# Kernel tuning notes

Measured on AMD Instinct MI355X. Metric: run time of the kernel, lower is better.

The kernel has to match this reference:

```python
import jax, jax.numpy as jnp
import numpy as np

B = 2; CIN = 64; COUT = 64; H = 192; W = 192
KH = 3; KW = 3; K = KH * KW; NC = 20
STRIDE = 1; PAD = 1; DIL = 1


def setup_inputs() -> dict:
    key = jax.random.key(0)
    ks = jax.random.split(key, 7)
    x = jax.random.normal(ks[0], (B, CIN, H, W), jnp.float32)
    input_LO = jax.random.uniform(ks[1], (B, NC, H, W), jnp.float32)
    output_LO = jax.random.uniform(ks[2], (B, NC, H, W), jnp.float32)  # HO=H, WO=W for k3 s1 p1
    weight = jax.random.normal(ks[3], (COUT, CIN, KH, KW), jnp.float32) * 0.05
    bias = jax.random.normal(ks[4], (COUT,), jnp.float32) * 0.05
    # conv_offset is zero-init in source; use small random weights so offsets are exercised
    off_w = jax.random.normal(ks[5], (2 * K, CIN, KH, KW), jnp.float32) * 0.01
    off_b = jnp.zeros((2 * K,), jnp.float32)
    return {"x": x, "input_LO": input_LO, "output_LO": output_LO,
            "weight": weight, "bias": bias, "off_w": off_w, "off_b": off_b}


def _gather(img_flat, idx):
    # img_flat: [B, C, H*W], idx: [B, N] -> [B, C, N]
    return jax.vmap(lambda im, ix: im[:, ix])(img_flat, idx)


def _bilinear(img, py, px, zero_pad):
    """Bilinear sample img [B,C,Hi,Wi] at pixel coords py/px [B,K,Ho,Wo].
    zero_pad=True -> zeros outside (deformable conv); False -> border clamp (grid_sample border)."""
    Bb, Cc, Hh, Ww = img.shape
    if not zero_pad:
        px = jnp.clip(px, 0.0, Ww - 1.0)
        py = jnp.clip(py, 0.0, Hh - 1.0)
    x0 = jnp.floor(px)
    y0 = jnp.floor(py)
    img_f = img.reshape(Bb, Cc, Hh * Ww)
    out = jnp.zeros((Bb, Cc) + px.shape[1:], img.dtype)
    for dy in (0.0, 1.0):
        for dx in (0.0, 1.0):
            yc = y0 + dy
            xc = x0 + dx
            w = (1.0 - jnp.abs(py - yc)) * (1.0 - jnp.abs(px - xc))
            if zero_pad:
                valid = (yc >= 0) & (yc <= Hh - 1) & (xc >= 0) & (xc <= Ww - 1)
                w = w * valid.astype(w.dtype)
            yi = jnp.clip(yc, 0, Hh - 1).astype(jnp.int32)
            xi = jnp.clip(xc, 0, Ww - 1).astype(jnp.int32)
            idx = (yi * Ww + xi).reshape(Bb, -1)
            g = _gather(img_f, idx).reshape((Bb, Cc) + px.shape[1:])
            out = out + g * w[:, None]
    return out


def reference(x, input_LO, output_LO, weight, bias, off_w, off_b):
    # 1) offset conv (torch chunk+cat is identity, so offset == conv_offset(x))
    offset = jax.lax.conv_general_dilated(
        x, off_w, (STRIDE, STRIDE), ((PAD, PAD), (PAD, PAD)),
        dimension_numbers=("NCHW", "OIHW", "NCHW")) + off_b[None, :, None, None]
    Bb, _, Ho, Wo = offset.shape
    off = offset.reshape(Bb, K, 2, Ho, Wo)
    off_y = off[:, :, 0]   # channel 2k   -> y offset
    off_x = off[:, :, 1]   # channel 2k+1 -> x offset
    hk = (jnp.arange(K) // KW).astype(x.dtype)[None, :, None, None]
    wk = (jnp.arange(K) % KW).astype(x.dtype)[None, :, None, None]

    # 2) mask: grid_sample label map at deformed locations (align_corners=True, border pad)
    hor = jnp.linspace(-1.0, 1.0, Wo)[None, None, None, :]
    ver = jnp.linspace(-1.0, 1.0, Ho)[None, None, :, None]
    gx = hor * STRIDE - PAD + (wk + off_x) / ((W - 1.0) / 2.0)
    gy = ver * STRIDE - PAD + (hk + off_y) / ((H - 1.0) / 2.0)
    px = (gx + 1.0) * (W - 1.0) / 2.0
    py = (gy + 1.0) * (H - 1.0) / 2.0
    samp_LO = _bilinear(input_LO, py, px, zero_pad=False)        # [B,NC,K,Ho,Wo]
    mask = jnp.einsum("bnkhw,bnhw->bkhw", samp_LO, output_LO)    # [B,K,Ho,Wo]

    # 3) modulated deformable conv (DCNv2 math, zero padding outside)
    base_y = (jnp.arange(Ho) * STRIDE - PAD).astype(x.dtype)[None, None, :, None]
    base_x = (jnp.arange(Wo) * STRIDE - PAD).astype(x.dtype)[None, None, None, :]
    py2 = base_y + hk * DIL + off_y
    px2 = base_x + wk * DIL + off_x
    samp = _bilinear(x, py2, px2, zero_pad=True)                 # [B,C,K,Ho,Wo]
    samp = samp * mask[:, None]
    out = jnp.einsum("bckhw,ock->bohw", samp, weight.reshape(COUT, CIN, K))
    return out + bias[None, :, None, None]
```

## Files before the change

### kernel.cpp

```cpp
#include <hip/hip_runtime.h>
#include <hip/hip_fp16.h>

#define Bn   2
#define CIN  64
#define COUT 64
#define Hd   192
#define Wd   192
#define HWd  (Hd*Wd)
#define Kk   9
#define NCh  20
#define NCP  24
#define NTILE 1152

typedef __attribute__((ext_vector_type(8))) short short8;
typedef __attribute__((ext_vector_type(4))) float f32x4;

static __device__ __forceinline__ ushort f2bf(float f) {
    unsigned u = __float_as_uint(f);
    u += 0x7fffu + ((u >> 16) & 1u);
    return (ushort)(u >> 16);
}
static __device__ __forceinline__ float bf2f(ushort v) {
    return __uint_as_float(((unsigned)v) << 16);
}
static __device__ __forceinline__ ushort f2h(float f) {
    return __half_as_ushort(__float2half_rn(f));
}
static __device__ __forceinline__ float h2f(ushort u) {
    return __half2float(__ushort_as_half(u));
}

__global__ __launch_bounds__(256) void kT(const float* __restrict__ x,
        const float* __restrict__ inLO, const float* __restrict__ outLO,
        const float* __restrict__ w, const float* __restrict__ off_w,
        ushort* __restrict__ xtb, ushort* __restrict__ inLOb,
        ushort* __restrict__ outLOb, ushort* __restrict__ wtb,
        ushort* __restrict__ owtb) {
    __shared__ float lds[20 * 257];
    int bid = blockIdx.x, tid = threadIdx.x;
    if (bid < 1152) {
        int b = bid / 576, p0 = (bid % 576) * 64;
        const float* src = x + b * CIN * HWd + p0;
        #pragma unroll
        for (int r = 0; r < 16; ++r) {
            int e = r * 256 + tid;
            int c = e >> 6, p = e & 63;
            lds[c * 65 + p] = src[c * HWd + p];
        }
        __syncthreads();
        ushort* dst = xtb + ((size_t)(b * HWd + p0)) * 64;
        #pragma unroll
        for (int r = 0; r < 16; ++r) {
            int e = r * 256 + tid;
            int p = e >> 6, c = e & 63;
            dst[e] = f2bf(lds[c * 65 + p]);
        }
    } else if (bid < 1728) {
        int q = bid - 1152;
        int t = q / 288; q %= 288;
        int b = q / 144, p0 = (q % 144) * 256;
        const float* src = (t == 0 ? inLO : outLO) + b * NCh * HWd + p0;
        ushort* dst = (t == 0 ? inLOb : outLOb) + ((size_t)(b * HWd + p0)) * NCP;
        #pragma unroll
        for (int r = 0; r < 20; ++r) {
            int e = r * 256 + tid;
            int n = e >> 8, p = e & 255;
            lds[n * 257 + p] = src[n * HWd + p];
        }
        __syncthreads();
        #pragma unroll
        for (int r = 0; r < 24; ++r) {
            int e = r * 256 + tid;
            int p = e / NCP, n = e - p * NCP;
            dst[e] = (n < NCh) ? f2bf(lds[n * 257 + p]) : (ushort)0;
        }
    } else if (bid < 1872) {
        int f = (bid - 1728) * 256 + tid;
        int e = f & 7, lane = (f >> 3) & 63;
        int kt = (f >> 9) & 1, nt = (f >> 10) & 3, tap = f >> 12;
        int o = nt * 16 + (lane & 15);
        int c = kt * 32 + (lane >> 4) * 8 + e;
        wtb[f] = f2bf(w[(o * CIN + c) * Kk + tap]);
    } else {
        int f = (bid - 1872) * 256 + tid;
        if (f < 18432) {
            int e = f & 7, lane = (f >> 3) & 63;
            int kt = (f >> 9) & 1, nt = (f >> 10) & 1, tap = f >> 11;
            int oc = nt * 16 + (lane & 15);
            int c = kt * 32 + (lane >> 4) * 8 + e;
            owtb[f] = (oc < 18) ? f2bf(off_w[(oc * CIN + c) * Kk + tap]) : (ushort)0;
        }
    }
}

__global__ __launch_bounds__(256) void k1_gemm(const ushort* __restrict__ xtb,
        const ushort* __restrict__ owtb, const float* __restrict__ off_b,
        float* __restrict__ off) {
    int tid = threadIdx.x, bid = blockIdx.x;
    int jt = bid % 3, i = (bid / 3) % Hd, b = bid / (3 * Hd);
    int j0 = jt * 64;
    int lane = tid & 63, wv = tid >> 6;
    int m = lane & 15;
    int ch8 = lane >> 4;
    int j = j0 + wv * 16 + m;
    const ushort* xb = xtb + (size_t)b * HWd * 64;

    float bv0 = off_b[m];
    float bv1 = (m < 2) ? off_b[16 + m] : 0.f;
    f32x4 acc0 = (f32x4){bv0, bv0, bv0, bv0};
    f32x4 acc1 = (f32x4){bv1, bv1, bv1, bv1};
    short8 zero8 = {0, 0, 0, 0, 0, 0, 0, 0};

    #pragma unroll
    for (int t = 0; t < 9; ++t) {
        int yy = i + t / 3 - 1;
        int xx = j + t % 3 - 1;
        bool ok = (yy >= 0) && (yy < Hd) && (xx >= 0) && (xx < Wd);
        int yc = min(max(yy, 0), Hd - 1), xc = min(max(xx, 0), Wd - 1);
        const ushort* rowp = xb + (size_t)(yc * Wd + xc) * 64 + ch8 * 8;
        short8 a0 = *(const short8*)rowp;
        short8 a1 = *(const short8*)(rowp + 32);
        a0 = ok ? a0 : zero8;
        a1 = ok ? a1 : zero8;
        const ushort* wb = owtb + ((size_t)t << 11);
        short8 b00 = *(const short8*)(wb + (lane << 3));
        short8 b01 = *(const short8*)(wb + 512 + (lane << 3));
        short8 b10 = *(const short8*)(wb + 1024 + (lane << 3));
        short8 b11 = *(const short8*)(wb + 1536 + (lane << 3));
        acc0 = __builtin_amdgcn_mfma_f32_16x16x32_bf16(a0, b00, acc0, 0, 0, 0);
        acc0 = __builtin_amdgcn_mfma_f32_16x16x32_bf16(a1, b01, acc0, 0, 0, 0);
        acc1 = __builtin_amdgcn_mfma_f32_16x16x32_bf16(a0, b10, acc1, 0, 0, 0);
        acc1 = __builtin_amdgcn_mfma_f32_16x16x32_bf16(a1, b11, acc1, 0, 0, 0);
    }

    int prow = j0 + wv * 16 + (lane >> 4) * 4;
    int oc = lane & 15;
    float* ob = off + (size_t)b * 18 * HWd + i * Wd;
    #pragma unroll
    for (int r = 0; r < 4; ++r)
        ob[oc * HWd + prow + r] = acc0[r];
    if (oc < 2) {
        #pragma unroll
        for (int r = 0; r < 4; ++r)
            ob[(16 + oc) * HWd + prow + r] = acc1[r];
    }
}

__global__ __launch_bounds__(256) void k2_mask(const ushort* __restrict__ inLOb,
        const ushort* __restrict__ outLOb, const float* __restrict__ off,
        uint4* __restrict__ rec) {
    int t = blockIdx.x * 256 + threadIdx.x;
    int p = t % HWd;
    int k = (t / HWd) % Kk;
    int b = t / (Kk * HWd);
    int j = p % Wd, i = p / Wd;
    float offy = off[(b * 18 + 2 * k) * HWd + p];
    float offx = off[(b * 18 + 2 * k + 1) * HWd + p];

    float py = (float)(i + (k / 3)) + offy - 95.5f;
    float px = (float)(j + (k % 3)) + offx - 95.5f;
    py = fminf(fmaxf(py, 0.f), 191.f);
    px = fminf(fmaxf(px, 0.f), 191.f);
    float y0f = floorf(py), x0f = floorf(px);
    float ly = py - y0f, lx = px - x0f;
    int y0 = (int)y0f, x0 = (int)x0f;
    int y1 = min(y0 + 1, Hd - 1), x1 = min(x0 + 1, Wd - 1);
    float w00 = (1.f - ly) * (1.f - lx);
    float w01 = (1.f - ly) * lx;
    float w10 = ly * (1.f - lx);
    float w11 = ly * lx;
    const short8* L00 = (const short8*)(inLOb + (size_t)(b * HWd + y0 * Wd + x0) * NCP);
    const short8* L01 = (const short8*)(inLOb + (size_t)(b * HWd + y0 * Wd + x1) * NCP);
    const short8* L10 = (const short8*)(inLOb + (size_t)(b * HWd + y1 * Wd + x0) * NCP);
    const short8* L11 = (const short8*)(inLOb + (size_t)(b * HWd + y1 * Wd + x1) * NCP);
    const short8* O  = (const short8*)(outLOb + (size_t)(b * HWd + p) * NCP);
    float acc = 0.f;
    #pragma unroll
    for (int n3 = 0; n3 < 3; ++n3) {
        short8 a = L00[n3], bb = L01[n3], c = L10[n3], d = L11[n3], o = O[n3];
        #pragma unroll
        for (int e = 0; e < 8; ++e) {
            float s = w00 * bf2f((ushort)a[e]) + w01 * bf2f((ushort)bb[e])
                    + w10 * bf2f((ushort)c[e]) + w11 * bf2f((ushort)d[e]);
            acc += s * bf2f((ushort)o[e]);
        }
    }

    float py2 = (float)(i - 1 + (k / 3)) + offy;
    float px2 = (float)(j - 1 + (k % 3)) + offx;
    float y0f2 = floorf(py2), x0f2 = floorf(px2);
    float ly2 = py2 - y0f2, lx2 = px2 - x0f2;
    int yA = (int)y0f2, xA = (int)x0f2;
    int yB = yA + 1, xB = xA + 1;
    bool vy0 = (yA >= 0 && yA < Hd), vy1 = (yB >= 0 && yB < Hd);
    bool vx0 = (xA >= 0 && xA < Wd), vx1 = (xB >= 0 && xB < Wd);
    float W00 = (vy0 && vx0) ? (1.f - ly2) * (1.f - lx2) * acc : 0.f;
    float W01 = (vy0 && vx1) ? (1.f - ly2) * lx2 * acc : 0.f;
    float W10 = (vy1 && vx0) ? ly2 * (1.f - lx2) * acc : 0.f;
    float W11 = (vy1 && vx1) ? ly2 * lx2 * acc : 0.f;
    int y0c = min(max(yA, 0), Hd - 1), y1c = min(max(yB, 0), Hd - 1);
    int x0c = min(max(xA, 0), Wd - 1), x1c = min(max(xB, 0), Wd - 1);
    uint4 r;
    r.x = (unsigned)y0c | ((unsigned)y1c << 16);
    r.y = (unsigned)x0c | ((unsigned)x1c << 16);
    r.z = (unsigned)f2h(W00) | ((unsigned)f2h(W01) << 16);
    r.w = (unsigned)f2h(W10) | ((unsigned)f2h(W11) << 16);
    rec[(size_t)(b * Kk + k) * HWd + p] = r;
}

__global__ __launch_bounds__(256) void k3_part(const ushort* __restrict__ xtb,
        const uint4* __restrict__ rec, const ushort* __restrict__ wtb,
        ushort* __restrict__ part) {
    __shared__ __align__(16) ushort A_lds[4 * 2 * 64 * 8];
    int tid = threadIdx.x;
    int bid = blockIdx.x;
    int h = bid >= NTILE;
    int tb = bid - (h ? NTILE : 0);
    int t0 = h ? 5 : 0, t1 = h ? 9 : 5;
    int jt = tb % 3, i = (tb / 3) % Hd, b = tb / (3 * Hd);
    int j0 = jt * 64;

    int lane = tid & 63;
    int wv_id = tid >> 6;
    int wm = wv_id >> 1;
    int wn = wv_id & 1;

    int pxo = lane & 7;
    int chunk = lane >> 3;
    int kt_s = chunk >> 2;
    int ksub = chunk & 3;
    const ushort* xb = xtb + (size_t)b * HWd * 64;

    f32x4 acc[2][2];
    #pragma unroll
    for (int mi = 0; mi < 2; ++mi)
        #pragma unroll
        for (int ni = 0; ni < 2; ++ni)
            acc[mi][ni] = (f32x4){0.f, 0.f, 0.f, 0.f};

    for (int t = t0; t < t1; ++t) {
        short8 bf[2][2];
        #pragma unroll
        for (int kt = 0; kt < 2; ++kt)
            #pragma unroll
            for (int ni = 0; ni < 2; ++ni) {
                int nt = wn * 2 + ni;
                bf[kt][ni] = *(const short8*)(wtb +
                    ((((t * 4 + nt) * 2 + kt) * 64 + lane) << 3));
            }

        const uint4* recb = rec + (size_t)(b * Kk + t) * HWd + i * Wd + j0;
        #pragma unroll
        for (int r = 0; r < 2; ++r) {
            int px_loc = (wv_id << 4) + (r << 3) + pxo;
            uint4 rc = recb[px_loc];
            int y0 = rc.x & 0xffff, y1 = rc.x >> 16;
            int x0 = rc.y & 0xffff, x1 = rc.y >> 16;
            float w00 = h2f((ushort)(rc.z & 0xffff));
            float w01 = h2f((ushort)(rc.z >> 16));
            float w10 = h2f((ushort)(rc.w & 0xffff));
            float w11 = h2f((ushort)(rc.w >> 16));
            const short8* g0p = (const short8*)(xb + (size_t)(y0 * Wd + x0) * 64 + chunk * 8);
            const short8* g1p = (const short8*)(xb + (size_t)(y0 * Wd + x1) * 64 + chunk * 8);
            const short8* g2p = (const short8*)(xb + (size_t)(y1 * Wd + x0) * 64 + chunk * 8);
            const short8* g3p = (const short8*)(xb + (size_t)(y1 * Wd + x1) * 64 + chunk * 8);
            short8 g0 = *g0p, g1 = *g1p, g2 = *g2p, g3 = *g3p;
            short8 pk;
            #pragma unroll
            for (int e = 0; e < 8; ++e) {
                float s = w00 * bf2f((ushort)g0[e]) + w01 * bf2f((ushort)g1[e])
                        + w10 * bf2f((ushort)g2[e]) + w11 * bf2f((ushort)g3[e]);
                pk[e] = (short)f2bf(s);
            }
            *(short8*)&A_lds[(((wv_id * 2 + kt_s) * 64 + ksub * 16 +
                               ((r << 3) + pxo)) << 3)] = pk;
        }
        __syncthreads();

        #pragma unroll
        for (int kt = 0; kt < 2; ++kt) {
            #pragma unroll
            for (int mi = 0; mi < 2; ++mi) {
                int mt2 = wm * 2 + mi;
                short8 af = *(const short8*)&A_lds[(((mt2 * 2 + kt) * 64 + lane) << 3)];
                acc[mi][0] = __builtin_amdgcn_mfma_f32_16x16x32_bf16(
                                 af, bf[kt][0], acc[mi][0], 0, 0, 0);
                acc[mi][1] = __builtin_amdgcn_mfma_f32_16x16x32_bf16(
                                 af, bf[kt][1], acc[mi][1], 0, 0, 0);
            }
        }
        __syncthreads();
    }

    ushort* pb = part + ((size_t)(h * NTILE + tb) << 12);
    int colo = lane & 15;
    int rb = (lane >> 4) * 4;
    #pragma unroll
    for (int ni = 0; ni < 2; ++ni) {
        int o = wn * 32 + ni * 16 + colo;
        #pragma unroll
        for (int mi = 0; mi < 2; ++mi) {
            int p0 = wm * 32 + mi * 16 + rb;
            ushort4 s;
            s.x = f2bf(acc[mi][ni][0]);
            s.y = f2bf(acc[mi][ni][1]);
            s.z = f2bf(acc[mi][ni][2]);
            s.w = f2bf(acc[mi][ni][3]);
            *(ushort4*)(pb + o * 64 + p0) = s;
        }
    }
}

__global__ __launch_bounds__(256) void k4_reduce(const ushort* __restrict__ part,
        const float* __restrict__ bias, float* __restrict__ out) {
    int g = blockIdx.x * 256 + threadIdx.x;
    int tile = g >> 9;
    int wi = g & 511;
    int o = wi >> 3;
    int p0 = (wi & 7) << 3;
    const short8* pp = (const short8*)part;
    short8 a = pp[g];
    short8 c = pp[g + NTILE * 512];
    float bv = bias[o];
    int jt = tile % 3, i = (tile / 3) % Hd, b = tile / (3 * Hd);
    float* op = out + ((size_t)(b * COUT + o) * HWd) + i * Wd + jt * 64 + p0;
    float4 r0, r1;
    r0.x = bf2f((ushort)a[0]) + bf2f((ushort)c[0]) + bv;
    r0.y = bf2f((ushort)a[1]) + bf2f((ushort)c[1]) + bv;
    r0.z = bf2f((ushort)a[2]) + bf2f((ushort)c[2]) + bv;
    r0.w = bf2f((ushort)a[3]) + bf2f((ushort)c[3]) + bv;
    r1.x = bf2f((ushort)a[4]) + bf2f((ushort)c[4]) + bv;
    r1.y = bf2f((ushort)a[5]) + bf2f((ushort)c[5]) + bv;
    r1.z = bf2f((ushort)a[6]) + bf2f((ushort)c[6]) + bv;
    r1.w = bf2f((ushort)a[7]) + bf2f((ushort)c[7]) + bv;
    *(float4*)op = r0;
    *(float4*)(op + 4) = r1;
}

extern "C" void kernel_launch(void* const* d_in, const int* in_sizes, int n_in,
                              void* d_out, int out_size, void* d_ws, size_t ws_size,
                              hipStream_t stream) {
    const float* x      = (const float*)d_in[0];
    const float* inLO   = (const float*)d_in[1];
    const float* outLO  = (const float*)d_in[2];
    const float* weight = (const float*)d_in[3];
    const float* bias   = (const float*)d_in[4];
    const float* off_w  = (const float*)d_in[5];
    const float* off_b  = (const float*)d_in[6];
    float* out = (float*)d_out;

    uint4*  rec    = (uint4*)d_ws;
    ushort* part   = (ushort*)(rec + (size_t)Bn * Kk * HWd);
    float*  off    = (float*)(part + (size_t)2 * NTILE * 4096);
    ushort* wtb    = (ushort*)(off + (size_t)Bn * 18 * HWd);
    ushort* owtb   = wtb + 36864;
    ushort* xtb    = owtb + 18432;
    ushort* inLOb  = xtb + (size_t)Bn * HWd * CIN;
    ushort* outLOb = inLOb + (size_t)Bn * HWd * NCP;

    kT<<<1944, 256, 0, stream>>>(x, inLO, outLO, weight, off_w,
                                 xtb, inLOb, outLOb, wtb, owtb);
    k1_gemm<<<NTILE, 256, 0, stream>>>(xtb, owtb, off_b, off);
    k2_mask<<<2592, 256, 0, stream>>>(inLOb, outLOb, off, rec);
    k3_part<<<2 * NTILE, 256, 0, stream>>>(xtb, rec, wtb, part);
    k4_reduce<<<2304, 256, 0, stream>>>(part, bias, out);
}
```

Before: 173.7 us.

## Feed MFMA A-fragments directly from registers, removing LDS staging and barriers

Restructures the k3_part deformable-conv GEMM so each wave owns 16 pixels and all 64 output channels. Every lane builds its bilinear-sampled bf16 A-fragments in registers in the MFMA input layout, which removes the LDS buffer and both __syncthreads per tap. Each wave now loads all four weight N-tiles per tap instead of two, so weight reads from global/L2 double. It also adds a launch-bounds occupancy hint of 4 blocks per CU.

```diff
diff --git a/kernel.cpp b/kernel.cpp
--- a/kernel.cpp
+++ b/kernel.cpp
@@ -208,10 +208,9 @@
     rec[(size_t)(b * Kk + k) * HWd + p] = r;
 }
 
-__global__ __launch_bounds__(256) void k3_part(const ushort* __restrict__ xtb,
+__global__ __launch_bounds__(256, 4) void k3_part(const ushort* __restrict__ xtb,
         const uint4* __restrict__ rec, const ushort* __restrict__ wtb,
         ushort* __restrict__ part) {
-    __shared__ __align__(16) ushort A_lds[4 * 2 * 64 * 8];
     int tid = threadIdx.x;
     int bid = blockIdx.x;
     int h = bid >= NTILE;
@@ -221,50 +220,37 @@
     int j0 = jt * 64;
 
     int lane = tid & 63;
-    int wv_id = tid >> 6;
-    int wm = wv_id >> 1;
-    int wn = wv_id & 1;
-
-    int pxo = lane & 7;
-    int chunk = lane >> 3;
-    int kt_s = chunk >> 2;
-    int ksub = chunk & 3;
+    int wv = tid >> 6;
+    int px16 = lane & 15;
+    int kg = lane >> 4;
     const ushort* xb = xtb + (size_t)b * HWd * 64;
 
-    f32x4 acc[2][2];
-    #pragma unroll
-    for (int mi = 0; mi < 2; ++mi)
-        #pragma unroll
-        for (int ni = 0; ni < 2; ++ni)
-            acc[mi][ni] = (f32x4){0.f, 0.f, 0.f, 0.f};
+    f32x4 acc[4];
+    #pragma unroll
+    for (int nt = 0; nt < 4; ++nt) acc[nt] = (f32x4){0.f, 0.f, 0.f, 0.f};
 
     for (int t = t0; t < t1; ++t) {
-        short8 bf[2][2];
-        #pragma unroll
-        for (int kt = 0; kt < 2; ++kt)
-            #pragma unroll
-            for (int ni = 0; ni < 2; ++ni) {
-                int nt = wn * 2 + ni;
-                bf[kt][ni] = *(const short8*)(wtb +
-                    ((((t * 4 + nt) * 2 + kt) * 64 + lane) << 3));
-            }
-
-        const uint4* recb = rec + (size_t)(b * Kk + t) * HWd + i * Wd + j0;
-        #pragma unroll
-        for (int r = 0; r < 2; ++r) {
-            int px_loc = (wv_id << 4) + (r << 3) + pxo;
-            uint4 rc = recb[px_loc];
-            int y0 = rc.x & 0xffff, y1 = rc.x >> 16;
-            int x0 = rc.y & 0xffff, x1 = rc.y >> 16;
-            float w00 = h2f((ushort)(rc.z & 0xffff));
-            float w01 = h2f((ushort)(rc.z >> 16));
-            float w10 = h2f((ushort)(rc.w & 0xffff));
-            float w11 = h2f((ushort)(rc.w >> 16));
-            const short8* g0p = (const short8*)(xb + (size_t)(y0 * Wd + x0) * 64 + chunk * 8);
-            const short8* g1p = (const short8*)(xb + (size_t)(y0 * Wd + x1) * 64 + chunk * 8);
-            const short8* g2p = (const short8*)(xb + (size_t)(y1 * Wd + x0) * 64 + chunk * 8);
-            const short8* g3p = (const short8*)(xb + (size_t)(y1 * Wd + x1) * 64 + chunk * 8);
-            short8 g0 = *g0p, g1 = *g1p, g2 = *g2p, g3 = *g3p;
+        const uint4* recb = rec + (size_t)(b * Kk + t) * HWd + i * Wd + j0 + wv * 16;
+        uint4 rc = recb[px16];
+        int y0 = rc.x & 0xffff, y1 = rc.x >> 16;
+        int x0 = rc.y & 0xffff, x1 = rc.y >> 16;
+        float w00 = h2f((ushort)(rc.z & 0xffff));
+        float w01 = h2f((ushort)(rc.z >> 16));
+        float w10 = h2f((ushort)(rc.w & 0xffff));
+        float w11 = h2f((ushort)(rc.w >> 16));
+        size_t r00 = (size_t)(y0 * Wd + x0) * 64;
+        size_t r01 = (size_t)(y0 * Wd + x1) * 64;
+        size_t r10 = (size_t)(y1 * Wd + x0) * 64;
+        size_t r11 = (size_t)(y1 * Wd + x1) * 64;
+
+        short8 af[2];
+        #pragma unroll
+        for (int kt = 0; kt < 2; ++kt) {
+            int co = kt * 32 + kg * 8;
+            short8 g0 = *(const short8*)(xb + r00 + co);
+            short8 g1 = *(const short8*)(xb + r01 + co);
+            short8 g2 = *(const short8*)(xb + r10 + co);
+            short8 g3 = *(const short8*)(xb + r11 + co);
             short8 pk;
             #pragma unroll
             for (int e = 0; e < 8; ++e) {
@@ -272,42 +258,30 @@
                         + w10 * bf2f((ushort)g2[e]) + w11 * bf2f((ushort)g3[e]);
                 pk[e] = (short)f2bf(s);
             }
-            *(short8*)&A_lds[(((wv_id * 2 + kt_s) * 64 + ksub * 16 +
-                               ((r << 3) + pxo)) << 3)] = pk;
-        }
-        __syncthreads();
-
-        #pragma unroll
-        for (int kt = 0; kt < 2; ++kt) {
-            #pragma unroll
-            for (int mi = 0; mi < 2; ++mi) {
-                int mt2 = wm * 2 + mi;
-                short8 af = *(const short8*)&A_lds[(((mt2 * 2 + kt) * 64 + lane) << 3)];
-                acc[mi][0] = __builtin_amdgcn_mfma_f32_16x16x32_bf16(
-                                 af, bf[kt][0], acc[mi][0], 0, 0, 0);
-                acc[mi][1] = __builtin_amdgcn_mfma_f32_16x16x32_bf16(
-                                 af, bf[kt][1], acc[mi][1], 0, 0, 0);
-            }
-        }
-        __syncthreads();
+            af[kt] = pk;
+        }
+
+        #pragma unroll
+        for (int nt = 0; nt < 4; ++nt) {
+            short8 b0 = *(const short8*)(wtb + ((((t * 4 + nt) * 2 + 0) * 64 + lane) << 3));
+            short8 b1 = *(const short8*)(wtb + ((((t * 4 + nt) * 2 + 1) * 64 + lane) << 3));
+            acc[nt] = __builtin_amdgcn_mfma_f32_16x16x32_bf16(af[0], b0, acc[nt], 0, 0, 0);
+            acc[nt] = __builtin_amdgcn_mfma_f32_16x16x32_bf16(af[1], b1, acc[nt], 0, 0, 0);
+        }
     }
 
     ushort* pb = part + ((size_t)(h * NTILE + tb) << 12);
     int colo = lane & 15;
-    int rb = (lane >> 4) * 4;
-    #pragma unroll
-    for (int ni = 0; ni < 2; ++ni) {
-        int o = wn * 32 + ni * 16 + colo;
-        #pragma unroll
-        for (int mi = 0; mi < 2; ++mi) {
-            int p0 = wm * 32 + mi * 16 + rb;
-            ushort4 s;
-            s.x = f2bf(acc[mi][ni][0]);
-            s.y = f2bf(acc[mi][ni][1]);
-            s.z = f2bf(acc[mi][ni][2]);
-            s.w = f2bf(acc[mi][ni][3]);
-            *(ushort4*)(pb + o * 64 + p0) = s;
-        }
+    int p0 = wv * 16 + (lane >> 4) * 4;
+    #pragma unroll
+    for (int nt = 0; nt < 4; ++nt) {
+        int o = nt * 16 + colo;
+        ushort4 s;
+        s.x = f2bf(acc[nt][0]);
+        s.y = f2bf(acc[nt][1]);
+        s.z = f2bf(acc[nt][2]);
+        s.w = f2bf(acc[nt][3]);
+        *(ushort4*)(pb + o * 64 + p0) = s;
     }
 }
 
```

After: 177.4 us. 1.02x slower.
